# Performance work log

Hardware: AMD Instinct MI355X
Metric: run time of the kernel (lower is better)

## Reference

```python
import jax, jax.numpy as jnp
import numpy as np

N, E, IN_FT, OUT_FT = 16384, 8192, 64, 64


def setup_inputs() -> dict:
    key = jax.random.key(0)
    k1, k2, k3, k4, k5 = jax.random.split(key, 5)
    stdv = 1.0 / np.sqrt(OUT_FT)
    x = jax.random.normal(k1, (N, IN_FT), dtype=jnp.float32)
    H = jax.random.uniform(k2, (N, E), dtype=jnp.float32)  # dense incidence, strictly positive
    W = jax.random.uniform(k3, (E,), dtype=jnp.float32)    # per-hyperedge weights
    weight = jax.random.uniform(k4, (IN_FT, OUT_FT), dtype=jnp.float32, minval=-stdv, maxval=stdv)
    bias = jax.random.uniform(k5, (OUT_FT,), dtype=jnp.float32, minval=-stdv, maxval=stdv)
    return {"x": x, "H": H, "W": W, "weight": weight, "bias": bias}


def reference(x, H, W, weight, bias):
    # out = DV^{-1/2} H diag(W) DE^{-1} H^T DV^{-1/2} x @ weight + bias
    # Diagonal matmuls of the original are expressed as broadcast scalings (same math).
    dv = jnp.sum(H, axis=1) ** -0.5   # [N]
    de = jnp.sum(H, axis=0) ** -1.0   # [E]
    x = x @ weight                            # [N, out_ft]
    x = de[:, None] * (H.T @ (dv[:, None] * x))  # invDE @ H^T @ DV2 @ x -> [E, out_ft]
    x = W[:, None] * x                        # diag(W) @ x
    x = dv[:, None] * (H @ x)                 # DV2 @ H @ x -> [N, out_ft]
    return x + bias
```

## Files before the change

### kernel.cpp

```cpp
#include <hip/hip_runtime.h>
#include <stdint.h>

#define NN 16384
#define EE 8192
#define FT 64

typedef float v4f __attribute__((ext_vector_type(4)));

__device__ __forceinline__ uint32_t prm(uint32_t hi, uint32_t lo, uint32_t sel) {
  return __builtin_amdgcn_perm(hi, lo, sel);
}

__device__ __forceinline__ uint32_t pk4(float a, float b, float c, float d) {
  uint32_t lo = __builtin_amdgcn_cvt_pk_fp8_f32(a, b, 0, false);
  return __builtin_amdgcn_cvt_pk_fp8_f32(c, d, lo, true);
}

__device__ __forceinline__ void gl_lds16(const uint8_t* g, uint8_t* l) {
  __builtin_amdgcn_global_load_lds(
      (const __attribute__((address_space(1))) void*)g,
      (__attribute__((address_space(3))) void*)l, 16, 0, 0);
}

__global__ __launch_bounds__(256) void k_prep_h(
    const float* __restrict__ H,
    uint8_t* __restrict__ Hn8,
    uint8_t* __restrict__ H8T,
    float* __restrict__ rowsum,
    float* __restrict__ colsum)
{
  __shared__ uint8_t T8[256 * 68];
  __shared__ float csumL[256];

  const int t    = threadIdx.x;
  const int lane = t & 63;
  const int wv   = t >> 6;
  const int e0   = blockIdx.x * 256;
  const int n0   = blockIdx.y * 64;

  csumL[t] = 0.f;
  __syncthreads();

  float cs0 = 0.f, cs1 = 0.f, cs2 = 0.f, cs3 = 0.f;

  for (int m = 0; m < 4; ++m) {
    const int g = wv + 4 * m;
    float4 r[4];
#pragma unroll
    for (int i = 0; i < 4; ++i) {
      const float* p = H + (size_t)(n0 + 4 * g + i) * EE + e0 + 4 * lane;
      r[i] = *(const float4*)p;
    }
    uint32_t D[4];
#pragma unroll
    for (int i = 0; i < 4; ++i) {
      cs0 += r[i].x; cs1 += r[i].y; cs2 += r[i].z; cs3 += r[i].w;
      float rsv = r[i].x + r[i].y + r[i].z + r[i].w;
#pragma unroll
      for (int s = 1; s < 64; s <<= 1) rsv += __shfl_xor(rsv, s);
      if (lane == 0) atomicAdd(&rowsum[n0 + 4 * g + i], rsv);
      D[i] = pk4(r[i].x, r[i].y, r[i].z, r[i].w);
      *(uint32_t*)(Hn8 + (size_t)(n0 + 4 * g + i) * EE + e0 + 4 * lane) = D[i];
    }
    uint32_t lo01 = prm(D[1], D[0], 0x05010400u);
    uint32_t hi01 = prm(D[1], D[0], 0x07030602u);
    uint32_t lo23 = prm(D[3], D[2], 0x05010400u);
    uint32_t hi23 = prm(D[3], D[2], 0x07030602u);
    uint32_t T0 = prm(lo23, lo01, 0x05040100u);
    uint32_t T1 = prm(lo23, lo01, 0x07060302u);
    uint32_t T2 = prm(hi23, hi01, 0x05040100u);
    uint32_t T3 = prm(hi23, hi01, 0x07060302u);
    *(uint32_t*)&T8[(size_t)(4 * lane + 0) * 68 + 4 * g] = T0;
    *(uint32_t*)&T8[(size_t)(4 * lane + 1) * 68 + 4 * g] = T1;
    *(uint32_t*)&T8[(size_t)(4 * lane + 2) * 68 + 4 * g] = T2;
    *(uint32_t*)&T8[(size_t)(4 * lane + 3) * 68 + 4 * g] = T3;
  }

  atomicAdd(&csumL[4 * lane + 0], cs0);
  atomicAdd(&csumL[4 * lane + 1], cs1);
  atomicAdd(&csumL[4 * lane + 2], cs2);
  atomicAdd(&csumL[4 * lane + 3], cs3);
  __syncthreads();
  atomicAdd(&colsum[e0 + t], csumL[t]);

  const int ec = t >> 2;
  const int nc = (t & 3) * 16;
#pragma unroll
  for (int jj = 0; jj < 4; ++jj) {
    const int el = ec + 64 * jj;
    uint4 v = *(const uint4*)&T8[(size_t)el * 68 + nc];
    *(uint4*)(H8T + (size_t)(e0 + el) * NN + n0 + nc) = v;
  }
}

__global__ __launch_bounds__(256) void k_z(
    const float* __restrict__ x,
    const float* __restrict__ weight,
    const float* __restrict__ rowsum,
    uint8_t* __restrict__ Zt)
{
  __shared__ float wT[64 * 68];
  const int t  = threadIdx.x;
  const int n0 = blockIdx.x * 64;
  for (int i = t; i < 4096; i += 256) {
    int cc = i >> 6, ff = i & 63;
    wT[ff * 68 + cc] = weight[i];
  }
  __syncthreads();

  const int f  = t >> 2;
  const int ns = (t & 3) * 16;

  float wr[64];
#pragma unroll
  for (int j = 0; j < 16; ++j) {
    float4 w4 = *(const float4*)&wT[f * 68 + 4 * j];
    wr[4*j] = w4.x; wr[4*j+1] = w4.y; wr[4*j+2] = w4.z; wr[4*j+3] = w4.w;
  }

  uint32_t outd[4];
#pragma unroll
  for (int i4 = 0; i4 < 4; ++i4) {
    float vb[4];
#pragma unroll
    for (int ii = 0; ii < 4; ++ii) {
      int n = n0 + ns + i4 * 4 + ii;
      const float4* xr = (const float4*)(x + (size_t)n * 64);
      float acc = 0.f;
#pragma unroll
      for (int j = 0; j < 16; ++j) {
        float4 xv = xr[j];
        acc += xv.x * wr[4*j] + xv.y * wr[4*j+1] + xv.z * wr[4*j+2] + xv.w * wr[4*j+3];
      }
      vb[ii] = 64.f * rsqrtf(rowsum[n]) * acc;
    }
    outd[i4] = pk4(vb[0], vb[1], vb[2], vb[3]);
  }
  uint4 v; v.x = outd[0]; v.y = outd[1]; v.z = outd[2]; v.w = outd[3];
  *(uint4*)(Zt + (size_t)f * NN + n0 + ns) = v;
}

__global__ __launch_bounds__(256) void k_gemm2(
    const uint8_t* __restrict__ A,
    const uint8_t* __restrict__ B,
    float* __restrict__ Out,
    int M, int K, int kchunk)
{
  __shared__ uint8_t Al[128 * 256];
  __shared__ uint8_t Bl[64 * 256];

  const int t    = threadIdx.x;
  const int lane = t & 63;
  const int wv   = t >> 6;
  const int m0   = blockIdx.x * 128;
  const int k0   = blockIdx.y * kchunk;
  const int iters = kchunk >> 8;

  const int r = lane & 15;
  const int q = lane >> 4;

  const int lr = lane >> 4;
  const int sl = lane & 15;

  const uint8_t* aptr[8];
  const uint8_t* bptr[4];
  uint8_t* aldst[8];
  uint8_t* bldst[4];
#pragma unroll
  for (int i = 0; i < 8; ++i) {
    int rA = wv * 32 + i * 4 + lr;
    int c  = sl ^ (rA & 7);
    aptr[i]  = A + (size_t)(m0 + rA) * K + k0 + c * 16;
    aldst[i] = &Al[(wv * 32 + i * 4) * 256];
  }
#pragma unroll
  for (int i = 0; i < 4; ++i) {
    int rB = wv * 16 + i * 4 + lr;
    int c  = sl ^ (rB & 7);
    bptr[i]  = B + (size_t)rB * K + k0 + c * 16;
    bldst[i] = &Bl[(wv * 16 + i * 4) * 256];
  }

  v4f acc[2][4];
#pragma unroll
  for (int mt = 0; mt < 2; ++mt)
#pragma unroll
    for (int ft = 0; ft < 4; ++ft)
      acc[mt][ft] = (v4f){0.f, 0.f, 0.f, 0.f};

  for (int kt = 0; kt < iters; ++kt) {
    __syncthreads();
    const size_t ko = (size_t)kt * 256;
#pragma unroll
    for (int i = 0; i < 8; ++i) gl_lds16(aptr[i] + ko, aldst[i]);
#pragma unroll
    for (int i = 0; i < 4; ++i) gl_lds16(bptr[i] + ko, bldst[i]);
    __syncthreads();
#pragma unroll
    for (int ks = 0; ks < 8; ++ks) {
      const int ch = ks * 2 + (q >> 1);
      const int h8 = (q & 1) * 8;
      long bfr[4], afr[2];
#pragma unroll
      for (int ft = 0; ft < 4; ++ft) {
        int rb = ft * 16 + r;
        bfr[ft] = *(const long*)&Bl[rb * 256 + ((ch ^ (rb & 7)) * 16) + h8];
      }
#pragma unroll
      for (int mt = 0; mt < 2; ++mt) {
        int ra = wv * 32 + mt * 16 + r;
        afr[mt] = *(const long*)&Al[ra * 256 + ((ch ^ (ra & 7)) * 16) + h8];
      }
#pragma unroll
      for (int mt = 0; mt < 2; ++mt)
#pragma unroll
        for (int ft = 0; ft < 4; ++ft)
          acc[mt][ft] = __builtin_amdgcn_mfma_f32_16x16x32_fp8_fp8(
              afr[mt], bfr[ft], acc[mt][ft], 0, 0, 0);
    }
  }

  float* U = Out + (size_t)blockIdx.y * M * 64;
#pragma unroll
  for (int mt = 0; mt < 2; ++mt)
#pragma unroll
    for (int ft = 0; ft < 4; ++ft)
#pragma unroll
      for (int i = 0; i < 4; ++i)
        U[(size_t)(m0 + wv * 32 + mt * 16 + 4 * q + i) * 64 + ft * 16 + r] =
            acc[mt][ft][i];
}

__global__ __launch_bounds__(256) void k_y(
    const float* __restrict__ Upart,
    const float* __restrict__ W,
    const float* __restrict__ colsum,
    uint8_t* __restrict__ Yt)
{
  __shared__ uint8_t TY[64 * 80];
  const int t  = threadIdx.x;
  const int e0 = blockIdx.x * 64;
  const int el = t >> 2;
  const int c4 = (t & 3) * 16;
  const int e  = e0 + el;
  const float sc = 128.f * W[e] / colsum[e];

  float s[16];
#pragma unroll
  for (int j = 0; j < 16; ++j) s[j] = 0.f;
  for (int p = 0; p < 8; ++p) {
    const float4* u = (const float4*)(Upart + ((size_t)p * EE + e) * 64 + c4);
#pragma unroll
    for (int j = 0; j < 4; ++j) {
      float4 a = u[j];
      s[4*j+0] += a.x; s[4*j+1] += a.y; s[4*j+2] += a.z; s[4*j+3] += a.w;
    }
  }
#pragma unroll
  for (int j = 0; j < 4; ++j) {
    uint32_t dw = pk4(sc * s[4*j], sc * s[4*j+1], sc * s[4*j+2], sc * s[4*j+3]);
    TY[(size_t)(c4 + 4 * j + 0) * 80 + el] = (uint8_t)(dw);
    TY[(size_t)(c4 + 4 * j + 1) * 80 + el] = (uint8_t)(dw >> 8);
    TY[(size_t)(c4 + 4 * j + 2) * 80 + el] = (uint8_t)(dw >> 16);
    TY[(size_t)(c4 + 4 * j + 3) * 80 + el] = (uint8_t)(dw >> 24);
  }
  __syncthreads();
  const int f  = t >> 2;
  const int ec = (t & 3) * 16;
  uint4 v = *(const uint4*)&TY[(size_t)f * 80 + ec];
  *(uint4*)(Yt + (size_t)f * EE + e0 + ec) = v;
}

__global__ __launch_bounds__(256) void k_out(
    const float* __restrict__ Vpart,
    const float* __restrict__ rowsum,
    const float* __restrict__ bias,
    float* __restrict__ out)
{
  const int t  = threadIdx.x;
  const int n  = blockIdx.x * 64 + (t >> 2);
  const int c4 = (t & 3) * 16;
  float s[16];
#pragma unroll
  for (int j = 0; j < 16; ++j) s[j] = 0.f;
#pragma unroll
  for (int p = 0; p < 4; ++p) {
    const float4* v = (const float4*)(Vpart + ((size_t)p * NN + n) * 64 + c4);
#pragma unroll
    for (int j = 0; j < 4; ++j) {
      float4 a = v[j];
      s[4*j+0] += a.x; s[4*j+1] += a.y; s[4*j+2] += a.z; s[4*j+3] += a.w;
    }
  }
  const float dv = rsqrtf(rowsum[n]) * (1.f / 8192.f);
  float4* o = (float4*)(out + (size_t)n * 64 + c4);
#pragma unroll
  for (int j = 0; j < 4; ++j) {
    float4 bb = *(const float4*)(bias + c4 + 4 * j);
    float4 rr;
    rr.x = s[4*j+0] * dv + bb.x;
    rr.y = s[4*j+1] * dv + bb.y;
    rr.z = s[4*j+2] * dv + bb.z;
    rr.w = s[4*j+3] * dv + bb.w;
    o[j] = rr;
  }
}

extern "C" void kernel_launch(void* const* d_in, const int* in_sizes, int n_in,
                              void* d_out, int out_size, void* d_ws, size_t ws_size,
                              hipStream_t stream) {
  const float* x      = (const float*)d_in[0];
  const float* H      = (const float*)d_in[1];
  const float* W      = (const float*)d_in[2];
  const float* weight = (const float*)d_in[3];
  const float* bias   = (const float*)d_in[4];
  float* out          = (float*)d_out;

  uint8_t* ws    = (uint8_t*)d_ws;
  uint8_t* Hn8   = ws;
  uint8_t* H8T   = ws + (size_t)NN * EE;
  float*  rowsum = (float*)(ws + 2ull * NN * EE);
  float*  colsum = rowsum + NN;
  uint8_t* Zt    = (uint8_t*)(colsum + EE);
  uint8_t* Yt    = Zt + (size_t)64 * NN;
  float*  Upart  = (float*)(Yt + (size_t)64 * EE);
  float*  Vpart  = Upart + 8ull * EE * 64;

  hipMemsetAsync(rowsum, 0, (NN + EE) * sizeof(float), stream);

  k_prep_h<<<dim3(32, 256), 256, 0, stream>>>(H, Hn8, H8T, rowsum, colsum);
  k_z<<<dim3(256), 256, 0, stream>>>(x, weight, rowsum, Zt);
  k_gemm2<<<dim3(64, 8), 256, 0, stream>>>(H8T, Zt, Upart, EE, NN, NN / 8);
  k_y<<<dim3(128), 256, 0, stream>>>(Upart, W, colsum, Yt);
  k_gemm2<<<dim3(128, 4), 256, 0, stream>>>(Hn8, Yt, Vpart, NN, EE, EE / 4);
  k_out<<<dim3(256), 256, 0, stream>>>(Vpart, rowsum, bias, out);
}
```

Before: 847.7 us.

## Double-buffer GEMM LDS tiles, raise split-K, and reduce row sums via LDS

The fp8 MFMA GEMM now uses two 128-wide K tiles in LDS and prefetches the next tile while computing the current one, replacing the load-sync-compute loop. Split-K is doubled for both GEMMs to launch more blocks, and the partial-sum reduction kernels read twice as many partials. In the H prep kernel, the 64-lane shuffle reduction and per-row global atomic are replaced by a 4-lane shuffle plus an LDS partial table summed by 64 threads. The cost is larger partial buffers in workspace and more reduction traffic.

```diff
diff --git a/kernel.cpp b/kernel.cpp
--- a/kernel.cpp
+++ b/kernel.cpp
@@ -31,6 +31,7 @@
 {
   __shared__ uint8_t T8[256 * 68];
   __shared__ float csumL[256];
+  __shared__ float rpart[64][17];
 
   const int t    = threadIdx.x;
   const int lane = t & 63;
@@ -56,9 +57,9 @@
     for (int i = 0; i < 4; ++i) {
       cs0 += r[i].x; cs1 += r[i].y; cs2 += r[i].z; cs3 += r[i].w;
       float rsv = r[i].x + r[i].y + r[i].z + r[i].w;
-#pragma unroll
-      for (int s = 1; s < 64; s <<= 1) rsv += __shfl_xor(rsv, s);
-      if (lane == 0) atomicAdd(&rowsum[n0 + 4 * g + i], rsv);
+      rsv += __shfl_xor(rsv, 1);
+      rsv += __shfl_xor(rsv, 2);
+      if ((lane & 3) == 0) rpart[4 * g + i][lane >> 2] = rsv;
       D[i] = pk4(r[i].x, r[i].y, r[i].z, r[i].w);
       *(uint32_t*)(Hn8 + (size_t)(n0 + 4 * g + i) * EE + e0 + 4 * lane) = D[i];
     }
@@ -83,6 +84,13 @@
   __syncthreads();
   atomicAdd(&colsum[e0 + t], csumL[t]);
 
+  if (t < 64) {
+    float s = 0.f;
+#pragma unroll
+    for (int j = 0; j < 16; ++j) s += rpart[t][j];
+    atomicAdd(&rowsum[n0 + t], s);
+  }
+
   const int ec = t >> 2;
   const int nc = (t & 3) * 16;
 #pragma unroll
@@ -146,39 +154,41 @@
     float* __restrict__ Out,
     int M, int K, int kchunk)
 {
-  __shared__ uint8_t Al[128 * 256];
-  __shared__ uint8_t Bl[64 * 256];
+  __shared__ uint8_t Al[2][128 * 128];
+  __shared__ uint8_t Bl[2][64 * 128];
 
   const int t    = threadIdx.x;
   const int lane = t & 63;
   const int wv   = t >> 6;
   const int m0   = blockIdx.x * 128;
   const int k0   = blockIdx.y * kchunk;
-  const int iters = kchunk >> 8;
+  const int iters = kchunk >> 7;
 
   const int r = lane & 15;
   const int q = lane >> 4;
 
-  const int lr = lane >> 4;
-  const int sl = lane & 15;
-
-  const uint8_t* aptr[8];
-  const uint8_t* bptr[4];
-  uint8_t* aldst[8];
-  uint8_t* bldst[4];
-#pragma unroll
-  for (int i = 0; i < 8; ++i) {
-    int rA = wv * 32 + i * 4 + lr;
+  const int lr = lane >> 3;
+  const int sl = lane & 7;
+
+  const uint8_t* aptr[4];
+  const uint8_t* bptr[2];
+  uint32_t aoff[4];
+  uint32_t boff[2];
+#pragma unroll
+  for (int i = 0; i < 4; ++i) {
+    int ga = i * 4 + wv;
+    int rA = ga * 8 + lr;
     int c  = sl ^ (rA & 7);
-    aptr[i]  = A + (size_t)(m0 + rA) * K + k0 + c * 16;
-    aldst[i] = &Al[(wv * 32 + i * 4) * 256];
-  }
-#pragma unroll
-  for (int i = 0; i < 4; ++i) {
-    int rB = wv * 16 + i * 4 + lr;
+    aptr[i] = A + (size_t)(m0 + rA) * K + k0 + c * 16;
+    aoff[i] = ga * 1024;
+  }
+#pragma unroll
+  for (int i = 0; i < 2; ++i) {
+    int gb = i * 4 + wv;
+    int rB = gb * 8 + lr;
     int c  = sl ^ (rB & 7);
-    bptr[i]  = B + (size_t)rB * K + k0 + c * 16;
-    bldst[i] = &Bl[(wv * 16 + i * 4) * 256];
+    bptr[i] = B + (size_t)rB * K + k0 + c * 16;
+    boff[i] = gb * 1024;
   }
 
   v4f acc[2][4];
@@ -188,28 +198,37 @@
     for (int ft = 0; ft < 4; ++ft)
       acc[mt][ft] = (v4f){0.f, 0.f, 0.f, 0.f};
 
+#pragma unroll
+  for (int i = 0; i < 4; ++i) gl_lds16(aptr[i], &Al[0][aoff[i]]);
+#pragma unroll
+  for (int i = 0; i < 2; ++i) gl_lds16(bptr[i], &Bl[0][boff[i]]);
+  __syncthreads();
+
+  int cur = 0;
   for (int kt = 0; kt < iters; ++kt) {
-    __syncthreads();
-    const size_t ko = (size_t)kt * 256;
-#pragma unroll
-    for (int i = 0; i < 8; ++i) gl_lds16(aptr[i] + ko, aldst[i]);
-#pragma unroll
-    for (int i = 0; i < 4; ++i) gl_lds16(bptr[i] + ko, bldst[i]);
-    __syncthreads();
-#pragma unroll
-    for (int ks = 0; ks < 8; ++ks) {
+    if (kt + 1 < iters) {
+      const size_t ko = (size_t)(kt + 1) * 128;
+#pragma unroll
+      for (int i = 0; i < 4; ++i) gl_lds16(aptr[i] + ko, &Al[cur ^ 1][aoff[i]]);
+#pragma unroll
+      for (int i = 0; i < 2; ++i) gl_lds16(bptr[i] + ko, &Bl[cur ^ 1][boff[i]]);
+    }
+    const uint8_t* Ab = Al[cur];
+    const uint8_t* Bb = Bl[cur];
+#pragma unroll
+    for (int ks = 0; ks < 4; ++ks) {
       const int ch = ks * 2 + (q >> 1);
       const int h8 = (q & 1) * 8;
       long bfr[4], afr[2];
 #pragma unroll
       for (int ft = 0; ft < 4; ++ft) {
         int rb = ft * 16 + r;
-        bfr[ft] = *(const long*)&Bl[rb * 256 + ((ch ^ (rb & 7)) * 16) + h8];
+        bfr[ft] = *(const long*)&Bb[rb * 128 + ((ch ^ (rb & 7)) * 16) + h8];
       }
 #pragma unroll
       for (int mt = 0; mt < 2; ++mt) {
         int ra = wv * 32 + mt * 16 + r;
-        afr[mt] = *(const long*)&Al[ra * 256 + ((ch ^ (ra & 7)) * 16) + h8];
+        afr[mt] = *(const long*)&Ab[ra * 128 + ((ch ^ (ra & 7)) * 16) + h8];
       }
 #pragma unroll
       for (int mt = 0; mt < 2; ++mt)
@@ -218,6 +237,8 @@
           acc[mt][ft] = __builtin_amdgcn_mfma_f32_16x16x32_fp8_fp8(
               afr[mt], bfr[ft], acc[mt][ft], 0, 0, 0);
     }
+    __syncthreads();
+    cur ^= 1;
   }
 
   float* U = Out + (size_t)blockIdx.y * M * 64;
@@ -248,7 +269,7 @@
   float s[16];
 #pragma unroll
   for (int j = 0; j < 16; ++j) s[j] = 0.f;
-  for (int p = 0; p < 8; ++p) {
+  for (int p = 0; p < 16; ++p) {
     const float4* u = (const float4*)(Upart + ((size_t)p * EE + e) * 64 + c4);
 #pragma unroll
     for (int j = 0; j < 4; ++j) {
@@ -284,7 +305,7 @@
 #pragma unroll
   for (int j = 0; j < 16; ++j) s[j] = 0.f;
 #pragma unroll
-  for (int p = 0; p < 4; ++p) {
+  for (int p = 0; p < 8; ++p) {
     const float4* v = (const float4*)(Vpart + ((size_t)p * NN + n) * 64 + c4);
 #pragma unroll
     for (int j = 0; j < 4; ++j) {
@@ -324,14 +345,14 @@
   uint8_t* Zt    = (uint8_t*)(colsum + EE);
   uint8_t* Yt    = Zt + (size_t)64 * NN;
   float*  Upart  = (float*)(Yt + (size_t)64 * EE);
-  float*  Vpart  = Upart + 8ull * EE * 64;
+  float*  Vpart  = Upart + 16ull * EE * 64;
 
   hipMemsetAsync(rowsum, 0, (NN + EE) * sizeof(float), stream);
 
   k_prep_h<<<dim3(32, 256), 256, 0, stream>>>(H, Hn8, H8T, rowsum, colsum);
   k_z<<<dim3(256), 256, 0, stream>>>(x, weight, rowsum, Zt);
-  k_gemm2<<<dim3(64, 8), 256, 0, stream>>>(H8T, Zt, Upart, EE, NN, NN / 8);
+  k_gemm2<<<dim3(64, 16), 256, 0, stream>>>(H8T, Zt, Upart, EE, NN, NN / 16);
   k_y<<<dim3(128), 256, 0, stream>>>(Upart, W, colsum, Yt);
-  k_gemm2<<<dim3(128, 4), 256, 0, stream>>>(Hn8, Yt, Vpart, NN, EE, EE / 4);
+  k_gemm2<<<dim3(128, 8), 256, 0, stream>>>(Hn8, Yt, Vpart, NN, EE, EE / 8);
   k_out<<<dim3(256), 256, 0, stream>>>(Vpart, rowsum, bias, out);
 }
```

New measurement: 879.9 us. 1.04x slower.
